# Kernel tuning notes

Measured on AMD Instinct MI355X. Metric: run time of the kernel, lower is better.

## Reference

```python
import jax, jax.numpy as jnp
import numpy as np

N = 500000
E = 1000000
B = 16384
F_IN, H, D = 82, 128, 256


def setup_inputs() -> dict:
    key = jax.random.key(0)
    ks = jax.random.split(key, 12)
    x = jax.random.normal(ks[0], (N, F_IN), dtype=jnp.float32)
    edge_index = jax.random.randint(ks[1], (2, E), 0, N, dtype=jnp.int64)
    batch = jnp.sort(jax.random.randint(ks[2], (N,), 0, B, dtype=jnp.int64))
    s = 0.05
    return {
        "x": x,
        "edge_index": edge_index,
        "batch": batch,
        "W0": jax.random.normal(ks[3], (F_IN, H), dtype=jnp.float32) * s,
        "b0": jnp.zeros((H,), dtype=jnp.float32),
        "W1": jax.random.normal(ks[4], (H, H), dtype=jnp.float32) * s,
        "b1": jnp.zeros((H,), dtype=jnp.float32),
        "W2": jax.random.normal(ks[5], (H, H), dtype=jnp.float32) * s,
        "b2": jnp.zeros((H,), dtype=jnp.float32),
        "gate_w": jax.random.normal(ks[6], (H, 1), dtype=jnp.float32) * s,
        "gate_b": jnp.zeros((1,), dtype=jnp.float32),
        "proj_w": jax.random.normal(ks[7], (H, D), dtype=jnp.float32) * s,
        "proj_b": jnp.zeros((D,), dtype=jnp.float32),
    }


def _gcn_conv(x, src, dst, norm, W, b):
    # PyG GCNConv: linear transform, gather from src, scale by sym-norm, scatter-add to dst
    h = x @ W  # (N, out)
    msg = h[src] * norm[:, None]  # (E+N, out)
    out = jax.ops.segment_sum(msg, dst, num_segments=N)
    return out + b


def reference(x, edge_index, batch, W0, b0, W1, b1, W2, b2, gate_w, gate_b, proj_w, proj_b):
    # add self-loops (GCNConv default add_self_loops=True)
    loop = jnp.arange(N, dtype=edge_index.dtype)
    src = jnp.concatenate([edge_index[0], loop])
    dst = jnp.concatenate([edge_index[1], loop])
    # symmetric normalization: deg computed on target (col) with unit edge weights
    deg = jax.ops.segment_sum(jnp.ones_like(dst, dtype=x.dtype), dst, num_segments=N)
    dis = jnp.where(deg > 0, jax.lax.rsqrt(jnp.maximum(deg, 1.0)), 0.0)
    norm = dis[src] * dis[dst]  # (E+N,)

    h = jax.nn.relu(_gcn_conv(x, src, dst, norm, W0, b0))
    h = jax.nn.relu(_gcn_conv(h, src, dst, norm, W1, b1))
    h = jax.nn.relu(_gcn_conv(h, src, dst, norm, W2, b2))

    # GlobalAttention pooling: segment softmax over gate scores, weighted scatter-sum
    gate = (h @ gate_w + gate_b)[:, 0]  # (N,)
    m = jax.ops.segment_max(gate, batch, num_segments=B)
    e = jnp.exp(gate - m[batch])
    denom = jax.ops.segment_sum(e, batch, num_segments=B)
    alpha = e / denom[batch]  # (N,)
    graph_emb = jax.ops.segment_sum(alpha[:, None] * h, batch, num_segments=B)  # (B, H)

    return graph_emb @ proj_w + proj_b  # (B, D)
```

## Files before the change

kernel.cpp:

```cpp
#include <hip/hip_runtime.h>
#include <hip/hip_bf16.h>
#include <cstdint>


typedef __attribute__((ext_vector_type(8))) short short8;
typedef __attribute__((ext_vector_type(4))) float f32x4;

__device__ __forceinline__ float b2f(unsigned int hi16) {
    return __builtin_bit_cast(float, hi16);
}
__device__ __forceinline__ unsigned short f2b(float f) {
    unsigned int u = __builtin_bit_cast(unsigned int, f);
    u += 0x7fffu + ((u >> 16) & 1u);
    return (unsigned short)(u >> 16);
}
__device__ __forceinline__ unsigned int packbf(float lo, float hi) {
    return ((unsigned int)f2b(hi) << 16) | f2b(lo);
}

__global__ void k_count(const int* __restrict__ dst, int* __restrict__ cnt, int E) {
    int e = blockIdx.x * blockDim.x + threadIdx.x;
    if (e < E) atomicAdd(&cnt[dst[e]], 1);
}

__global__ void k_scan1(const int* __restrict__ in, int* __restrict__ out1,
                        int* __restrict__ bsum, float* __restrict__ dis, int n) {
    __shared__ int s[256];
    int t = threadIdx.x;
    int base = blockIdx.x * 2048 + t * 8;
    int v[8];
    int run = 0;
#pragma unroll
    for (int i = 0; i < 8; ++i) {
        int idx = base + i;
        int x = (idx < n) ? in[idx] : 0;
        if (idx < n) dis[idx] = rsqrtf((float)x + 1.0f);
        run += x;
        v[i] = run;
    }
    s[t] = run;
    __syncthreads();
    for (int off = 1; off < 256; off <<= 1) {
        int add = (t >= off) ? s[t - off] : 0;
        __syncthreads();
        s[t] += add;
        __syncthreads();
    }
    int pre = (t > 0) ? s[t - 1] : 0;
#pragma unroll
    for (int i = 0; i < 8; ++i) {
        int idx = base + i;
        if (idx < n) out1[idx] = v[i] + pre;
    }
    if (t == 255) bsum[blockIdx.x] = s[255];
}

__global__ void k_scan2(int* bsum, int nb) {
    __shared__ int s[256];
    int t = threadIdx.x;
    s[t] = (t < nb) ? bsum[t] : 0;
    __syncthreads();
    for (int off = 1; off < 256; off <<= 1) {
        int add = (t >= off) ? s[t - off] : 0;
        __syncthreads();
        s[t] += add;
        __syncthreads();
    }
    if (t < nb) bsum[t] = s[t];
}

__global__ void k_scan3(int* __restrict__ rowstart, const int* __restrict__ bsum, int n) {
    int b = blockIdx.x, t = threadIdx.x;
    if (b == 0) {
        if (t == 0) rowstart[0] = 0;
        return;
    }
    int add = bsum[b - 1];
    int* out1 = rowstart + 1;
    int base = b * 2048 + t * 8;
#pragma unroll
    for (int i = 0; i < 8; ++i) {
        int idx = base + i;
        if (idx < n) out1[idx] += add;
    }
}

__global__ void k_fill(const int* __restrict__ src, const int* __restrict__ dst,
                       const int* __restrict__ rowstart, int* __restrict__ cur0,
                       int* __restrict__ csr_src, int E) {
    int e = blockIdx.x * blockDim.x + threadIdx.x;
    if (e >= E) return;
    int d = dst[e];
    int pos = rowstart[d] + atomicAdd(&cur0[d], 1);
    csr_src[pos] = src[e];
}

__global__ void k_cvtw3(const float* __restrict__ W0, const float* __restrict__ W1,
                        const float* __restrict__ W2, unsigned short* __restrict__ wp0,
                        unsigned short* __restrict__ wp1, unsigned short* __restrict__ wp2) {
    int tid = blockIdx.x * blockDim.x + threadIdx.x;
    const float* W;
    unsigned short* o;
    int Ksrc, f;
    if (tid < 3 * 512) { W = W0; o = wp0; Ksrc = 82; f = tid; }
    else if (tid < 7 * 512) { W = W1; o = wp1; Ksrc = 128; f = tid - 3 * 512; }
    else if (tid < 11 * 512) { W = W2; o = wp2; Ksrc = 128; f = tid - 7 * 512; }
    else return;
    int lane = f & 63, fr = f >> 6;
    int m = fr >> 3, ct = fr & 7;
    int col = ct * 16 + (lane & 15);
    int kb = m * 32 + ((lane >> 4) << 3);
    unsigned short v[8];
#pragma unroll
    for (int j = 0; j < 8; ++j) {
        int k = kb + j;
        v[j] = (k < Ksrc) ? f2b(W[k * 128 + col]) : (unsigned short)0;
    }
    *(short8*)(o + (size_t)f * 8) = *(short8*)v;
}

__global__ __launch_bounds__(256) void k_xd(const float* __restrict__ x,
                                            const float* __restrict__ dis,
                                            unsigned int* __restrict__ xd, int n) {
    int tid = blockIdx.x * blockDim.x + threadIdx.x;
    if (tid >= n * 48) return;
    int v = tid / 48;
    int c = (tid - v * 48) * 2;
    float dv = dis[v];
    const float* xv = x + (size_t)v * 82;
    float fx = (c < 82) ? dv * xv[c] : 0.f;
    float fy = (c + 1 < 82) ? dv * xv[c + 1] : 0.f;
    xd[tid] = packbf(fx, fy);
}

template <int KS, bool SCALE, bool GATE>
__global__ __launch_bounds__(256, 6) void k_fused(
    const unsigned int* __restrict__ hd, const float* __restrict__ dis,
    const int* __restrict__ rowstart, const int* __restrict__ csr,
    const unsigned short* __restrict__ Wp, const float* __restrict__ bias,
    unsigned short* __restrict__ out, const float* __restrict__ gw,
    const float* __restrict__ gb, float* __restrict__ gate, int n) {
    constexpr int RU = KS * 16;
    __shared__ unsigned int As[64 * 64];
    int t = threadIdx.x, lane = t & 63, w = t >> 6;
    int tile = blockIdx.x * 64;
    const bool act = (RU == 64) ? true : (lane < RU);
    const int li = act ? lane : 0;

    for (int g = 0; g < 4; ++g) {
        int r = (w << 4) + g * 4;
        int v0 = tile + r;
        unsigned int* dst0 = &As[(r + 0) * 64 + (lane ^ (((r + 0) & 7) << 2))];
        unsigned int* dst1 = &As[(r + 1) * 64 + (lane ^ (((r + 1) & 7) << 2))];
        unsigned int* dst2 = &As[(r + 2) * 64 + (lane ^ (((r + 2) & 7) << 2))];
        unsigned int* dst3 = &As[(r + 3) * 64 + (lane ^ (((r + 3) & 7) << 2))];
        if (v0 >= n) {
            *dst0 = 0u; *dst1 = 0u; *dst2 = 0u; *dst3 = 0u;
            continue;
        }
        int nv = n - v0;
        if (nv > 4) nv = 4;
        int e0 = rowstart[v0];
        int eE = rowstart[v0 + nv];
        int b1 = (nv > 1) ? rowstart[v0 + 1] : eE;
        int b2 = (nv > 2) ? rowstart[v0 + 2] : eE;
        int b3 = (nv > 3) ? rowstart[v0 + 3] : eE;

        unsigned int s0 = hd[(size_t)v0 * RU + li];
        unsigned int s1 = (nv > 1) ? hd[(size_t)(v0 + 1) * RU + li] : 0u;
        unsigned int s2 = (nv > 2) ? hd[(size_t)(v0 + 2) * RU + li] : 0u;
        unsigned int s3 = (nv > 3) ? hd[(size_t)(v0 + 3) * RU + li] : 0u;
        float a0x = b2f(s0 << 16), a0y = b2f(s0 & 0xffff0000u);
        float a1x = b2f(s1 << 16), a1y = b2f(s1 & 0xffff0000u);
        float a2x = b2f(s2 << 16), a2y = b2f(s2 & 0xffff0000u);
        float a3x = b2f(s3 << 16), a3y = b2f(s3 & 0xffff0000u);

        for (int e = e0; e < eE; e += 8) {
            int rem = eE - e;
            int i1 = (rem > 1) ? e + 1 : e;
            int i2 = (rem > 2) ? e + 2 : e;
            int i3 = (rem > 3) ? e + 3 : e;
            int i4 = (rem > 4) ? e + 4 : e;
            int i5 = (rem > 5) ? e + 5 : e;
            int i6 = (rem > 6) ? e + 6 : e;
            int i7 = (rem > 7) ? e + 7 : e;
            int u0 = csr[e],  u1 = csr[i1], u2 = csr[i2], u3 = csr[i3];
            int u4 = csr[i4], u5 = csr[i5], u6 = csr[i6], u7 = csr[i7];
            unsigned int r0v = hd[(size_t)u0 * RU + li];
            unsigned int r1v = hd[(size_t)u1 * RU + li];
            unsigned int r2v = hd[(size_t)u2 * RU + li];
            unsigned int r3v = hd[(size_t)u3 * RU + li];
            unsigned int r4v = hd[(size_t)u4 * RU + li];
            unsigned int r5v = hd[(size_t)u5 * RU + li];
            unsigned int r6v = hd[(size_t)u6 * RU + li];
            unsigned int r7v = hd[(size_t)u7 * RU + li];
#define ACC(rv, ei)                                                     \
            {                                                           \
                float fx = b2f((rv) << 16), fy = b2f((rv) & 0xffff0000u); \
                if ((ei) < b1) { a0x += fx; a0y += fy; }                \
                else if ((ei) < b2) { a1x += fx; a1y += fy; }           \
                else if ((ei) < b3) { a2x += fx; a2y += fy; }           \
                else { a3x += fx; a3y += fy; }                          \
            }
            ACC(r0v, e)
            if (rem > 1) ACC(r1v, e + 1)
            if (rem > 2) ACC(r2v, e + 2)
            if (rem > 3) ACC(r3v, e + 3)
            if (rem > 4) ACC(r4v, e + 4)
            if (rem > 5) ACC(r5v, e + 5)
            if (rem > 6) ACC(r6v, e + 6)
            if (rem > 7) ACC(r7v, e + 7)
#undef ACC
        }

        float d0 = dis[v0];
        float d1 = (nv > 1) ? dis[v0 + 1] : 0.f;
        float d2 = (nv > 2) ? dis[v0 + 2] : 0.f;
        float d3 = (nv > 3) ? dis[v0 + 3] : 0.f;
        *dst0 = act ? packbf(d0 * a0x, d0 * a0y) : 0u;
        *dst1 = (act && nv > 1) ? packbf(d1 * a1x, d1 * a1y) : 0u;
        *dst2 = (act && nv > 2) ? packbf(d2 * a2x, d2 * a2y) : 0u;
        *dst3 = (act && nv > 3) ? packbf(d3 * a3x, d3 * a3y) : 0u;
    }
    __syncthreads();

    int r0 = lane & 15, ch = lane >> 4;
    const unsigned int* arow = &As[((w << 4) + r0) << 6];
    f32x4 acc[8];
#pragma unroll
    for (int ct = 0; ct < 8; ++ct) acc[ct] = (f32x4){0.f, 0.f, 0.f, 0.f};
#pragma unroll
    for (int m = 0; m < KS; ++m) {
        int slot = (ch + 4 * m) ^ (r0 & 7);
        short8 a = *(const short8*)(arow + slot * 4);
        const short8* wf = (const short8*)Wp + ((size_t)(m * 8) * 64 + lane);
#pragma unroll
        for (int ct = 0; ct < 8; ++ct) {
            short8 b = wf[ct * 64];
            acc[ct] = __builtin_amdgcn_mfma_f32_16x16x32_bf16(a, b, acc[ct], 0, 0, 0);
        }
    }

    int cq = r0;
    float bb[8], gwv[8];
#pragma unroll
    for (int ct = 0; ct < 8; ++ct) {
        bb[ct] = bias[ct * 16 + cq];
        if (GATE) gwv[ct] = gw[ct * 16 + cq];
    }
    float gbv = GATE ? gb[0] : 0.f;
    int rbase = tile + (w << 4) + (ch << 2);
#pragma unroll
    for (int reg = 0; reg < 4; ++reg) {
        int row = rbase + reg;
        bool ok = row < n;
        float dv = (SCALE && ok) ? dis[row] : 1.f;
        float gp = 0.f;
#pragma unroll
        for (int ct = 0; ct < 8; ++ct) {
            float o = fmaxf(acc[ct][reg] + bb[ct], 0.f);
            if (GATE) gp = fmaf(o, gwv[ct], gp);
            if (ok) out[(size_t)row * 128 + ct * 16 + cq] = f2b(SCALE ? o * dv : o);
        }
        if (GATE) {
            gp += __shfl_xor(gp, 1);
            gp += __shfl_xor(gp, 2);
            gp += __shfl_xor(gp, 4);
            gp += __shfl_xor(gp, 8);
            if (cq == 0 && ok) gate[row] = gp + gbv;
        }
    }
}

__global__ __launch_bounds__(256) void k_pool(const unsigned short* __restrict__ h,
                                              const float* __restrict__ gate,
                                              const int* __restrict__ batch,
                                              float* __restrict__ emb, int n, int B) {
    int wid = (blockIdx.x * blockDim.x + threadIdx.x) >> 6;
    int lane = threadIdx.x & 63;
    if (wid >= B) return;
    int bnd = 0;
    if (lane < 2) {
        int g = wid + lane;
        int lo = 0, hi = n;
        while (lo < hi) {
            int mid = (lo + hi) >> 1;
            if (batch[mid] < g) lo = mid + 1;
            else hi = mid;
        }
        bnd = lo;
    }
    int s = __shfl(bnd, 0), e2 = __shfl(bnd, 1);
    float* ev2 = emb + (size_t)wid * 128 + lane * 2;
    if (s >= e2) {
        ev2[0] = 0.f;
        ev2[1] = 0.f;
        return;
    }
    float m = -INFINITY;
    for (int v = s + lane; v < e2; v += 64) m = fmaxf(m, gate[v]);
#pragma unroll
    for (int off = 32; off; off >>= 1) m = fmaxf(m, __shfl_xor(m, off));
    float a0 = 0.f, a1 = 0.f, den = 0.f;
    for (int v = s; v < e2; ++v) {
        float ev = __expf(gate[v] - m);
        den += ev;
        unsigned int hv = *(const unsigned int*)((const char*)h + (size_t)v * 256 + lane * 4);
        a0 = fmaf(ev, b2f(hv << 16), a0);
        a1 = fmaf(ev, b2f(hv & 0xffff0000u), a1);
    }
    float inv = 1.f / den;
    ev2[0] = a0 * inv;
    ev2[1] = a1 * inv;
}

__global__ __launch_bounds__(256) void k_proj(const float* __restrict__ emb,
                                              const float* __restrict__ pw,
                                              const float* __restrict__ pb,
                                              float* __restrict__ out, int B) {
    __shared__ float es[32][128];
    int g0 = blockIdx.x * 32;
    int t = threadIdx.x;
    for (int i = t; i < 1024; i += 256) {
        int g = g0 + (i >> 5);
        float4 val = (g < B) ? ((const float4*)emb)[(size_t)g * 32 + (i & 31)]
                             : make_float4(0.f, 0.f, 0.f, 0.f);
        *(float4*)&es[i >> 5][(i & 31) * 4] = val;
    }
    __syncthreads();
    float acc[32];
#pragma unroll
    for (int i = 0; i < 32; ++i) acc[i] = 0.f;
    for (int k = 0; k < 128; ++k) {
        float wv = pw[k * 256 + t];
#pragma unroll
        for (int i = 0; i < 32; ++i) acc[i] = fmaf(es[i][k], wv, acc[i]);
    }
    float b = pb[t];
#pragma unroll
    for (int i = 0; i < 32; ++i) {
        int g = g0 + i;
        if (g < B) out[(size_t)g * 256 + t] = acc[i] + b;
    }
}

extern "C" void kernel_launch(void* const* d_in, const int* in_sizes, int n_in,
                              void* d_out, int out_size, void* d_ws, size_t ws_size,
                              hipStream_t stream) {
    const float* x = (const float*)d_in[0];
    const int* ei = (const int*)d_in[1];
    const int* batch = (const int*)d_in[2];
    const float* W0 = (const float*)d_in[3];
    const float* b0 = (const float*)d_in[4];
    const float* W1 = (const float*)d_in[5];
    const float* b1 = (const float*)d_in[6];
    const float* W2 = (const float*)d_in[7];
    const float* b2 = (const float*)d_in[8];
    const float* gw = (const float*)d_in[9];
    const float* gb = (const float*)d_in[10];
    const float* pw = (const float*)d_in[11];
    const float* pb = (const float*)d_in[12];
    float* out = (float*)d_out;

    const int N = in_sizes[2];
    const int E = in_sizes[1] / 2;
    const int B = out_size / 256;
    (void)n_in;

    const int* esrc = ei;
    const int* edst = ei + E;

    char* p = (char*)d_ws;
    auto carve = [&](size_t bytes) {
        char* r = p;
        p += (bytes + 255) & ~(size_t)255;
        return r;
    };
    unsigned int* xd = (unsigned int*)carve((size_t)N * 48 * 4);
    unsigned int* hA = (unsigned int*)carve((size_t)N * 64 * 4);
    unsigned int* hB = (unsigned int*)carve((size_t)N * 64 * 4);
    float* emb = (float*)carve((size_t)B * 128 * 4);
    int* csr_src = (int*)carve((size_t)E * 4);
    float* dis = (float*)carve((size_t)N * 4);
    int* cnt = (int*)carve((size_t)2 * N * 4);
    int* cur0 = cnt + N;
    int* rowstart = (int*)carve((size_t)(N + 1) * 4);
    float* gate = (float*)carve((size_t)N * 4);
    int* bsum = (int*)carve((size_t)4096 * 4);
    unsigned short* wp0 = (unsigned short*)carve((size_t)3 * 512 * 8 * 2);
    unsigned short* wp1 = (unsigned short*)carve((size_t)4 * 512 * 8 * 2);
    unsigned short* wp2 = (unsigned short*)carve((size_t)4 * 512 * 8 * 2);
    if ((size_t)(p - (char*)d_ws) > ws_size) return;

    const int nb = (N + 2047) / 2048;

    hipMemsetAsync(cnt, 0, (size_t)2 * N * 4, stream);
    k_count<<<(E + 255) / 256, 256, 0, stream>>>(edst, cnt, E);
    k_scan1<<<nb, 256, 0, stream>>>(cnt, rowstart + 1, bsum, dis, N);
    k_scan2<<<1, 256, 0, stream>>>(bsum, nb);
    k_scan3<<<nb, 256, 0, stream>>>(rowstart, bsum, N);
    k_fill<<<(E + 255) / 256, 256, 0, stream>>>(esrc, edst, rowstart, cur0, csr_src, E);
    k_cvtw3<<<22, 256, 0, stream>>>(W0, W1, W2, wp0, wp1, wp2);
    k_xd<<<(N * 48 + 255) / 256, 256, 0, stream>>>(x, dis, xd, N);

    const int fb = (N + 63) / 64;

    k_fused<3, true, false><<<fb, 256, 0, stream>>>(
        xd, dis, rowstart, csr_src, wp0, b0, (unsigned short*)hA,
        nullptr, nullptr, nullptr, N);
    k_fused<4, true, false><<<fb, 256, 0, stream>>>(
        hA, dis, rowstart, csr_src, wp1, b1, (unsigned short*)hB,
        nullptr, nullptr, nullptr, N);
    k_fused<4, false, true><<<fb, 256, 0, stream>>>(
        hB, dis, rowstart, csr_src, wp2, b2, (unsigned short*)hA,
        gw, gb, gate, N);

    k_pool<<<(B + 3) / 4, 256, 0, stream>>>((const unsigned short*)hA, gate, batch,
                                            emb, N, B);
    k_proj<<<(B + 31) / 32, 256, 0, stream>>>(emb, pw, pb, out, B);
}
```

Before: 684.4 us.

## Fuse input scaling into first GCN layer and merge scan kernels

Removes the separate k_xd pre-pass: the first layer now gathers fp32 x rows directly and applies the per-source degree scale with fmaf, instead of reading a bf16 pre-scaled copy. This drops one full pass over x and the xd buffer, in exchange for wider fp32 gathers plus extra dis[] gathers per edge. k_scan2 is folded into k_scan3, with each block reducing the block sums itself, which removes one launch. Row starts and self features are prefetched into registers, and the later layers use launch bounds of 8 instead of 6, which adds register pressure.

```diff
diff --git a/kernel.cpp b/kernel.cpp
--- a/kernel.cpp
+++ b/kernel.cpp
@@ -55,27 +55,19 @@
     if (t == 255) bsum[blockIdx.x] = s[255];
 }
 
-__global__ void k_scan2(int* bsum, int nb) {
-    __shared__ int s[256];
-    int t = threadIdx.x;
-    s[t] = (t < nb) ? bsum[t] : 0;
-    __syncthreads();
-    for (int off = 1; off < 256; off <<= 1) {
-        int add = (t >= off) ? s[t - off] : 0;
-        __syncthreads();
-        s[t] += add;
-        __syncthreads();
-    }
-    if (t < nb) bsum[t] = s[t];
-}
-
 __global__ void k_scan3(int* __restrict__ rowstart, const int* __restrict__ bsum, int n) {
     int b = blockIdx.x, t = threadIdx.x;
     if (b == 0) {
         if (t == 0) rowstart[0] = 0;
         return;
     }
-    int add = bsum[b - 1];
+    __shared__ int ws[4];
+    int v = (t < b) ? bsum[t] : 0;
+#pragma unroll
+    for (int off = 32; off; off >>= 1) v += __shfl_xor(v, off);
+    if ((t & 63) == 0) ws[t >> 6] = v;
+    __syncthreads();
+    int add = ws[0] + ws[1] + ws[2] + ws[3];
     int* out1 = rowstart + 1;
     int base = b * 2048 + t * 8;
 #pragma unroll
@@ -119,34 +111,26 @@
     *(short8*)(o + (size_t)f * 8) = *(short8*)v;
 }
 
-__global__ __launch_bounds__(256) void k_xd(const float* __restrict__ x,
-                                            const float* __restrict__ dis,
-                                            unsigned int* __restrict__ xd, int n) {
-    int tid = blockIdx.x * blockDim.x + threadIdx.x;
-    if (tid >= n * 48) return;
-    int v = tid / 48;
-    int c = (tid - v * 48) * 2;
-    float dv = dis[v];
-    const float* xv = x + (size_t)v * 82;
-    float fx = (c < 82) ? dv * xv[c] : 0.f;
-    float fy = (c + 1 < 82) ? dv * xv[c + 1] : 0.f;
-    xd[tid] = packbf(fx, fy);
-}
-
-template <int KS, bool SCALE, bool GATE>
-__global__ __launch_bounds__(256, 6) void k_fused(
-    const unsigned int* __restrict__ hd, const float* __restrict__ dis,
+__global__ __launch_bounds__(256, 6) void k_fused0(
+    const float* __restrict__ x, const float* __restrict__ dis,
     const int* __restrict__ rowstart, const int* __restrict__ csr,
     const unsigned short* __restrict__ Wp, const float* __restrict__ bias,
-    unsigned short* __restrict__ out, const float* __restrict__ gw,
-    const float* __restrict__ gb, float* __restrict__ gate, int n) {
-    constexpr int RU = KS * 16;
+    unsigned short* __restrict__ out, int n) {
     __shared__ unsigned int As[64 * 64];
     int t = threadIdx.x, lane = t & 63, w = t >> 6;
     int tile = blockIdx.x * 64;
-    const bool act = (RU == 64) ? true : (lane < RU);
-    const int li = act ? lane : 0;
-
+    const bool act = lane < 41;
+    const int c0 = (act ? lane : 0) * 2;
+    int sbase = tile + (w << 4);
+
+    int bb[17];
+#pragma unroll
+    for (int i = 0; i < 17; ++i) {
+        int idx = sbase + i;
+        bb[i] = rowstart[idx < n ? idx : n];
+    }
+
+#pragma unroll
     for (int g = 0; g < 4; ++g) {
         int r = (w << 4) + g * 4;
         int v0 = tile + r;
@@ -154,26 +138,26 @@
         unsigned int* dst1 = &As[(r + 1) * 64 + (lane ^ (((r + 1) & 7) << 2))];
         unsigned int* dst2 = &As[(r + 2) * 64 + (lane ^ (((r + 2) & 7) << 2))];
         unsigned int* dst3 = &As[(r + 3) * 64 + (lane ^ (((r + 3) & 7) << 2))];
-        if (v0 >= n) {
+        int nv = n - v0;
+        nv = nv < 0 ? 0 : (nv > 4 ? 4 : nv);
+        if (nv == 0) {
             *dst0 = 0u; *dst1 = 0u; *dst2 = 0u; *dst3 = 0u;
             continue;
         }
-        int nv = n - v0;
-        if (nv > 4) nv = 4;
-        int e0 = rowstart[v0];
-        int eE = rowstart[v0 + nv];
-        int b1 = (nv > 1) ? rowstart[v0 + 1] : eE;
-        int b2 = (nv > 2) ? rowstart[v0 + 2] : eE;
-        int b3 = (nv > 3) ? rowstart[v0 + 3] : eE;
-
-        unsigned int s0 = hd[(size_t)v0 * RU + li];
-        unsigned int s1 = (nv > 1) ? hd[(size_t)(v0 + 1) * RU + li] : 0u;
-        unsigned int s2 = (nv > 2) ? hd[(size_t)(v0 + 2) * RU + li] : 0u;
-        unsigned int s3 = (nv > 3) ? hd[(size_t)(v0 + 3) * RU + li] : 0u;
-        float a0x = b2f(s0 << 16), a0y = b2f(s0 & 0xffff0000u);
-        float a1x = b2f(s1 << 16), a1y = b2f(s1 & 0xffff0000u);
-        float a2x = b2f(s2 << 16), a2y = b2f(s2 & 0xffff0000u);
-        float a3x = b2f(s3 << 16), a3y = b2f(s3 & 0xffff0000u);
+        int e0 = bb[g * 4], b1 = bb[g * 4 + 1], b2 = bb[g * 4 + 2],
+            b3 = bb[g * 4 + 3], eE = bb[g * 4 + 4];
+        int vc1 = (nv > 1) ? v0 + 1 : v0;
+        int vc2 = (nv > 2) ? v0 + 2 : v0;
+        int vc3 = (nv > 3) ? v0 + 3 : v0;
+        float2 t0 = *(const float2*)(x + (size_t)v0 * 82 + c0);
+        float2 t1 = *(const float2*)(x + (size_t)vc1 * 82 + c0);
+        float2 t2 = *(const float2*)(x + (size_t)vc2 * 82 + c0);
+        float2 t3 = *(const float2*)(x + (size_t)vc3 * 82 + c0);
+        float d0 = dis[v0], d1 = dis[vc1], d2 = dis[vc2], d3 = dis[vc3];
+        float a0x = d0 * t0.x, a0y = d0 * t0.y;
+        float a1x = d1 * t1.x, a1y = d1 * t1.y;
+        float a2x = d2 * t2.x, a2y = d2 * t2.y;
+        float a3x = d3 * t3.x, a3y = d3 * t3.y;
 
         for (int e = e0; e < eE; e += 8) {
             int rem = eE - e;
@@ -186,14 +170,137 @@
             int i7 = (rem > 7) ? e + 7 : e;
             int u0 = csr[e],  u1 = csr[i1], u2 = csr[i2], u3 = csr[i3];
             int u4 = csr[i4], u5 = csr[i5], u6 = csr[i6], u7 = csr[i7];
-            unsigned int r0v = hd[(size_t)u0 * RU + li];
-            unsigned int r1v = hd[(size_t)u1 * RU + li];
-            unsigned int r2v = hd[(size_t)u2 * RU + li];
-            unsigned int r3v = hd[(size_t)u3 * RU + li];
-            unsigned int r4v = hd[(size_t)u4 * RU + li];
-            unsigned int r5v = hd[(size_t)u5 * RU + li];
-            unsigned int r6v = hd[(size_t)u6 * RU + li];
-            unsigned int r7v = hd[(size_t)u7 * RU + li];
+            float2 r0 = *(const float2*)(x + (size_t)u0 * 82 + c0);
+            float2 r1 = *(const float2*)(x + (size_t)u1 * 82 + c0);
+            float2 r2 = *(const float2*)(x + (size_t)u2 * 82 + c0);
+            float2 r3 = *(const float2*)(x + (size_t)u3 * 82 + c0);
+            float2 r4 = *(const float2*)(x + (size_t)u4 * 82 + c0);
+            float2 r5 = *(const float2*)(x + (size_t)u5 * 82 + c0);
+            float2 r6 = *(const float2*)(x + (size_t)u6 * 82 + c0);
+            float2 r7 = *(const float2*)(x + (size_t)u7 * 82 + c0);
+            float du0 = dis[u0], du1 = dis[u1], du2 = dis[u2], du3 = dis[u3];
+            float du4 = dis[u4], du5 = dis[u5], du6 = dis[u6], du7 = dis[u7];
+#define ACC0(DU, RV, ei)                                                  \
+            {                                                             \
+                if ((ei) < b1) { a0x = fmaf(DU, RV.x, a0x); a0y = fmaf(DU, RV.y, a0y); } \
+                else if ((ei) < b2) { a1x = fmaf(DU, RV.x, a1x); a1y = fmaf(DU, RV.y, a1y); } \
+                else if ((ei) < b3) { a2x = fmaf(DU, RV.x, a2x); a2y = fmaf(DU, RV.y, a2y); } \
+                else { a3x = fmaf(DU, RV.x, a3x); a3y = fmaf(DU, RV.y, a3y); } \
+            }
+            ACC0(du0, r0, e)
+            if (rem > 1) ACC0(du1, r1, e + 1)
+            if (rem > 2) ACC0(du2, r2, e + 2)
+            if (rem > 3) ACC0(du3, r3, e + 3)
+            if (rem > 4) ACC0(du4, r4, e + 4)
+            if (rem > 5) ACC0(du5, r5, e + 5)
+            if (rem > 6) ACC0(du6, r6, e + 6)
+            if (rem > 7) ACC0(du7, r7, e + 7)
+#undef ACC0
+        }
+        *dst0 = act ? packbf(d0 * a0x, d0 * a0y) : 0u;
+        *dst1 = (act && nv > 1) ? packbf(d1 * a1x, d1 * a1y) : 0u;
+        *dst2 = (act && nv > 2) ? packbf(d2 * a2x, d2 * a2y) : 0u;
+        *dst3 = (act && nv > 3) ? packbf(d3 * a3x, d3 * a3y) : 0u;
+    }
+    __syncthreads();
+
+    int r0i = lane & 15, ch = lane >> 4;
+    const unsigned int* arow = &As[((w << 4) + r0i) << 6];
+    f32x4 acc[8];
+#pragma unroll
+    for (int ct = 0; ct < 8; ++ct) acc[ct] = (f32x4){0.f, 0.f, 0.f, 0.f};
+#pragma unroll
+    for (int m = 0; m < 3; ++m) {
+        int slot = (ch + 4 * m) ^ (r0i & 7);
+        short8 a = *(const short8*)(arow + slot * 4);
+        const short8* wf = (const short8*)Wp + ((size_t)(m * 8) * 64 + lane);
+#pragma unroll
+        for (int ct = 0; ct < 8; ++ct) {
+            short8 b = wf[ct * 64];
+            acc[ct] = __builtin_amdgcn_mfma_f32_16x16x32_bf16(a, b, acc[ct], 0, 0, 0);
+        }
+    }
+
+    float bbv[8];
+#pragma unroll
+    for (int ct = 0; ct < 8; ++ct) bbv[ct] = bias[ct * 16 + r0i];
+    int rbase = tile + (w << 4) + (ch << 2);
+#pragma unroll
+    for (int reg = 0; reg < 4; ++reg) {
+        int row = rbase + reg;
+        bool ok = row < n;
+        float dv = ok ? dis[row] : 1.f;
+#pragma unroll
+        for (int ct = 0; ct < 8; ++ct) {
+            float o = fmaxf(acc[ct][reg] + bbv[ct], 0.f);
+            if (ok) out[(size_t)row * 128 + ct * 16 + r0i] = f2b(o * dv);
+        }
+    }
+}
+
+template <bool SCALE, bool GATE>
+__global__ __launch_bounds__(256, 8) void k_fused(
+    const unsigned int* __restrict__ hd, const float* __restrict__ dis,
+    const int* __restrict__ rowstart, const int* __restrict__ csr,
+    const unsigned short* __restrict__ Wp, const float* __restrict__ bias,
+    unsigned short* __restrict__ out, const float* __restrict__ gw,
+    const float* __restrict__ gb, float* __restrict__ gate, int n) {
+    __shared__ unsigned int As[64 * 64];
+    int t = threadIdx.x, lane = t & 63, w = t >> 6;
+    int tile = blockIdx.x * 64;
+    int sbase = tile + (w << 4);
+
+    int bb[17];
+#pragma unroll
+    for (int i = 0; i < 17; ++i) {
+        int idx = sbase + i;
+        bb[i] = rowstart[idx < n ? idx : n];
+    }
+    unsigned int selfv[16];
+#pragma unroll
+    for (int i = 0; i < 16; ++i) {
+        int v = sbase + i;
+        int vc = (v < n) ? v : 0;
+        unsigned int val = hd[(size_t)vc * 64 + lane];
+        selfv[i] = (v < n) ? val : 0u;
+    }
+
+#pragma unroll
+    for (int g = 0; g < 4; ++g) {
+        int r = (w << 4) + g * 4;
+        int v0 = tile + r;
+        unsigned int* dst0 = &As[(r + 0) * 64 + (lane ^ (((r + 0) & 7) << 2))];
+        unsigned int* dst1 = &As[(r + 1) * 64 + (lane ^ (((r + 1) & 7) << 2))];
+        unsigned int* dst2 = &As[(r + 2) * 64 + (lane ^ (((r + 2) & 7) << 2))];
+        unsigned int* dst3 = &As[(r + 3) * 64 + (lane ^ (((r + 3) & 7) << 2))];
+        int nv = n - v0;
+        nv = nv < 0 ? 0 : (nv > 4 ? 4 : nv);
+        int e0 = bb[g * 4], b1 = bb[g * 4 + 1], b2 = bb[g * 4 + 2],
+            b3 = bb[g * 4 + 3], eE = bb[g * 4 + 4];
+        float a0x = b2f(selfv[g * 4 + 0] << 16), a0y = b2f(selfv[g * 4 + 0] & 0xffff0000u);
+        float a1x = b2f(selfv[g * 4 + 1] << 16), a1y = b2f(selfv[g * 4 + 1] & 0xffff0000u);
+        float a2x = b2f(selfv[g * 4 + 2] << 16), a2y = b2f(selfv[g * 4 + 2] & 0xffff0000u);
+        float a3x = b2f(selfv[g * 4 + 3] << 16), a3y = b2f(selfv[g * 4 + 3] & 0xffff0000u);
+
+        for (int e = e0; e < eE; e += 8) {
+            int rem = eE - e;
+            int i1 = (rem > 1) ? e + 1 : e;
+            int i2 = (rem > 2) ? e + 2 : e;
+            int i3 = (rem > 3) ? e + 3 : e;
+            int i4 = (rem > 4) ? e + 4 : e;
+            int i5 = (rem > 5) ? e + 5 : e;
+            int i6 = (rem > 6) ? e + 6 : e;
+            int i7 = (rem > 7) ? e + 7 : e;
+            int u0 = csr[e],  u1 = csr[i1], u2 = csr[i2], u3 = csr[i3];
+            int u4 = csr[i4], u5 = csr[i5], u6 = csr[i6], u7 = csr[i7];
+            unsigned int r0v = hd[(size_t)u0 * 64 + lane];
+            unsigned int r1v = hd[(size_t)u1 * 64 + lane];
+            unsigned int r2v = hd[(size_t)u2 * 64 + lane];
+            unsigned int r3v = hd[(size_t)u3 * 64 + lane];
+            unsigned int r4v = hd[(size_t)u4 * 64 + lane];
+            unsigned int r5v = hd[(size_t)u5 * 64 + lane];
+            unsigned int r6v = hd[(size_t)u6 * 64 + lane];
+            unsigned int r7v = hd[(size_t)u7 * 64 + lane];
 #define ACC(rv, ei)                                                     \
             {                                                           \
                 float fx = b2f((rv) << 16), fy = b2f((rv) & 0xffff0000u); \
@@ -213,25 +320,26 @@
 #undef ACC
         }
 
-        float d0 = dis[v0];
-        float d1 = (nv > 1) ? dis[v0 + 1] : 0.f;
-        float d2 = (nv > 2) ? dis[v0 + 2] : 0.f;
-        float d3 = (nv > 3) ? dis[v0 + 3] : 0.f;
-        *dst0 = act ? packbf(d0 * a0x, d0 * a0y) : 0u;
-        *dst1 = (act && nv > 1) ? packbf(d1 * a1x, d1 * a1y) : 0u;
-        *dst2 = (act && nv > 2) ? packbf(d2 * a2x, d2 * a2y) : 0u;
-        *dst3 = (act && nv > 3) ? packbf(d3 * a3x, d3 * a3y) : 0u;
+        int vc1 = (nv > 1) ? v0 + 1 : 0;
+        int vc2 = (nv > 2) ? v0 + 2 : 0;
+        int vc3 = (nv > 3) ? v0 + 3 : 0;
+        float d0 = dis[(nv > 0) ? v0 : 0];
+        float d1 = dis[vc1], d2 = dis[vc2], d3 = dis[vc3];
+        *dst0 = (nv > 0) ? packbf(d0 * a0x, d0 * a0y) : 0u;
+        *dst1 = (nv > 1) ? packbf(d1 * a1x, d1 * a1y) : 0u;
+        *dst2 = (nv > 2) ? packbf(d2 * a2x, d2 * a2y) : 0u;
+        *dst3 = (nv > 3) ? packbf(d3 * a3x, d3 * a3y) : 0u;
     }
     __syncthreads();
 
-    int r0 = lane & 15, ch = lane >> 4;
-    const unsigned int* arow = &As[((w << 4) + r0) << 6];
+    int r0i = lane & 15, ch = lane >> 4;
+    const unsigned int* arow = &As[((w << 4) + r0i) << 6];
     f32x4 acc[8];
 #pragma unroll
     for (int ct = 0; ct < 8; ++ct) acc[ct] = (f32x4){0.f, 0.f, 0.f, 0.f};
 #pragma unroll
-    for (int m = 0; m < KS; ++m) {
-        int slot = (ch + 4 * m) ^ (r0 & 7);
+    for (int m = 0; m < 4; ++m) {
+        int slot = (ch + 4 * m) ^ (r0i & 7);
         short8 a = *(const short8*)(arow + slot * 4);
         const short8* wf = (const short8*)Wp + ((size_t)(m * 8) * 64 + lane);
 #pragma unroll
@@ -241,12 +349,11 @@
         }
     }
 
-    int cq = r0;
-    float bb[8], gwv[8];
+    float bbv[8], gwv[8];
 #pragma unroll
     for (int ct = 0; ct < 8; ++ct) {
-        bb[ct] = bias[ct * 16 + cq];
-        if (GATE) gwv[ct] = gw[ct * 16 + cq];
+        bbv[ct] = bias[ct * 16 + r0i];
+        if (GATE) gwv[ct] = gw[ct * 16 + r0i];
     }
     float gbv = GATE ? gb[0] : 0.f;
     int rbase = tile + (w << 4) + (ch << 2);
@@ -258,16 +365,16 @@
         float gp = 0.f;
 #pragma unroll
         for (int ct = 0; ct < 8; ++ct) {
-            float o = fmaxf(acc[ct][reg] + bb[ct], 0.f);
+            float o = fmaxf(acc[ct][reg] + bbv[ct], 0.f);
             if (GATE) gp = fmaf(o, gwv[ct], gp);
-            if (ok) out[(size_t)row * 128 + ct * 16 + cq] = f2b(SCALE ? o * dv : o);
+            if (ok) out[(size_t)row * 128 + ct * 16 + r0i] = f2b(SCALE ? o * dv : o);
         }
         if (GATE) {
             gp += __shfl_xor(gp, 1);
             gp += __shfl_xor(gp, 2);
             gp += __shfl_xor(gp, 4);
             gp += __shfl_xor(gp, 8);
-            if (cq == 0 && ok) gate[row] = gp + gbv;
+            if (r0i == 0 && ok) gate[row] = gp + gbv;
         }
     }
 }
@@ -376,7 +483,6 @@
         p += (bytes + 255) & ~(size_t)255;
         return r;
     };
-    unsigned int* xd = (unsigned int*)carve((size_t)N * 48 * 4);
     unsigned int* hA = (unsigned int*)carve((size_t)N * 64 * 4);
     unsigned int* hB = (unsigned int*)carve((size_t)N * 64 * 4);
     float* emb = (float*)carve((size_t)B * 128 * 4);
@@ -397,21 +503,18 @@
     hipMemsetAsync(cnt, 0, (size_t)2 * N * 4, stream);
     k_count<<<(E + 255) / 256, 256, 0, stream>>>(edst, cnt, E);
     k_scan1<<<nb, 256, 0, stream>>>(cnt, rowstart + 1, bsum, dis, N);
-    k_scan2<<<1, 256, 0, stream>>>(bsum, nb);
     k_scan3<<<nb, 256, 0, stream>>>(rowstart, bsum, N);
     k_fill<<<(E + 255) / 256, 256, 0, stream>>>(esrc, edst, rowstart, cur0, csr_src, E);
     k_cvtw3<<<22, 256, 0, stream>>>(W0, W1, W2, wp0, wp1, wp2);
-    k_xd<<<(N * 48 + 255) / 256, 256, 0, stream>>>(x, dis, xd, N);
 
     const int fb = (N + 63) / 64;
 
-    k_fused<3, true, false><<<fb, 256, 0, stream>>>(
-        xd, dis, rowstart, csr_src, wp0, b0, (unsigned short*)hA,
-        nullptr, nullptr, nullptr, N);
-    k_fused<4, true, false><<<fb, 256, 0, stream>>>(
+    k_fused0<<<fb, 256, 0, stream>>>(x, dis, rowstart, csr_src, wp0, b0,
+                                     (unsigned short*)hA, N);
+    k_fused<true, false><<<fb, 256, 0, stream>>>(
         hA, dis, rowstart, csr_src, wp1, b1, (unsigned short*)hB,
         nullptr, nullptr, nullptr, N);
-    k_fused<4, false, true><<<fb, 256, 0, stream>>>(
+    k_fused<false, true><<<fb, 256, 0, stream>>>(
         hB, dis, rowstart, csr_src, wp2, b2, (unsigned short*)hA,
         gw, gb, gate, N);
 
```

Measured after the change: 827.7 us. 20.9% more time.

## Use single-wave blocks in fused GCN kernel, fold scan2 into scan3, unroll pooling

Applied to the files above, without the earlier changes.

The fused gather+MFMA kernel now runs one wave per block over 16 rows instead of four waves over 64 rows, dropping the block barrier and letting waves finish independently of slower siblings. The second scan pass is folded into the third by having each block reduce preceding block sums itself, removing a launch. The attention pooling loop is unrolled by four to overlap loads of gate and features. Smaller blocks mean more block scheduling and a different occupancy limit from the new launch bounds.

```diff
diff --git a/kernel.cpp b/kernel.cpp
--- a/kernel.cpp
+++ b/kernel.cpp
@@ -55,27 +55,19 @@
     if (t == 255) bsum[blockIdx.x] = s[255];
 }
 
-__global__ void k_scan2(int* bsum, int nb) {
-    __shared__ int s[256];
-    int t = threadIdx.x;
-    s[t] = (t < nb) ? bsum[t] : 0;
-    __syncthreads();
-    for (int off = 1; off < 256; off <<= 1) {
-        int add = (t >= off) ? s[t - off] : 0;
-        __syncthreads();
-        s[t] += add;
-        __syncthreads();
-    }
-    if (t < nb) bsum[t] = s[t];
-}
-
 __global__ void k_scan3(int* __restrict__ rowstart, const int* __restrict__ bsum, int n) {
     int b = blockIdx.x, t = threadIdx.x;
     if (b == 0) {
         if (t == 0) rowstart[0] = 0;
         return;
     }
-    int add = bsum[b - 1];
+    __shared__ int ws[4];
+    int v = (t < b) ? bsum[t] : 0;
+#pragma unroll
+    for (int off = 32; off; off >>= 1) v += __shfl_xor(v, off);
+    if ((t & 63) == 0) ws[t >> 6] = v;
+    __syncthreads();
+    int add = ws[0] + ws[1] + ws[2] + ws[3];
     int* out1 = rowstart + 1;
     int base = b * 2048 + t * 8;
 #pragma unroll
@@ -134,21 +126,21 @@
 }
 
 template <int KS, bool SCALE, bool GATE>
-__global__ __launch_bounds__(256, 6) void k_fused(
+__global__ __launch_bounds__(64, 8) void k_fused(
     const unsigned int* __restrict__ hd, const float* __restrict__ dis,
     const int* __restrict__ rowstart, const int* __restrict__ csr,
     const unsigned short* __restrict__ Wp, const float* __restrict__ bias,
     unsigned short* __restrict__ out, const float* __restrict__ gw,
     const float* __restrict__ gb, float* __restrict__ gate, int n) {
     constexpr int RU = KS * 16;
-    __shared__ unsigned int As[64 * 64];
-    int t = threadIdx.x, lane = t & 63, w = t >> 6;
-    int tile = blockIdx.x * 64;
+    __shared__ unsigned int As[16 * 64];
+    int lane = threadIdx.x & 63;
+    int tile = blockIdx.x * 16;
     const bool act = (RU == 64) ? true : (lane < RU);
     const int li = act ? lane : 0;
 
     for (int g = 0; g < 4; ++g) {
-        int r = (w << 4) + g * 4;
+        int r = g * 4;
         int v0 = tile + r;
         unsigned int* dst0 = &As[(r + 0) * 64 + (lane ^ (((r + 0) & 7) << 2))];
         unsigned int* dst1 = &As[(r + 1) * 64 + (lane ^ (((r + 1) & 7) << 2))];
@@ -222,10 +214,9 @@
         *dst2 = (act && nv > 2) ? packbf(d2 * a2x, d2 * a2y) : 0u;
         *dst3 = (act && nv > 3) ? packbf(d3 * a3x, d3 * a3y) : 0u;
     }
-    __syncthreads();
 
     int r0 = lane & 15, ch = lane >> 4;
-    const unsigned int* arow = &As[((w << 4) + r0) << 6];
+    const unsigned int* arow = &As[r0 << 6];
     f32x4 acc[8];
 #pragma unroll
     for (int ct = 0; ct < 8; ++ct) acc[ct] = (f32x4){0.f, 0.f, 0.f, 0.f};
@@ -241,15 +232,14 @@
         }
     }
 
-    int cq = r0;
     float bb[8], gwv[8];
 #pragma unroll
     for (int ct = 0; ct < 8; ++ct) {
-        bb[ct] = bias[ct * 16 + cq];
-        if (GATE) gwv[ct] = gw[ct * 16 + cq];
+        bb[ct] = bias[ct * 16 + r0];
+        if (GATE) gwv[ct] = gw[ct * 16 + r0];
     }
     float gbv = GATE ? gb[0] : 0.f;
-    int rbase = tile + (w << 4) + (ch << 2);
+    int rbase = tile + (ch << 2);
 #pragma unroll
     for (int reg = 0; reg < 4; ++reg) {
         int row = rbase + reg;
@@ -260,14 +250,14 @@
         for (int ct = 0; ct < 8; ++ct) {
             float o = fmaxf(acc[ct][reg] + bb[ct], 0.f);
             if (GATE) gp = fmaf(o, gwv[ct], gp);
-            if (ok) out[(size_t)row * 128 + ct * 16 + cq] = f2b(SCALE ? o * dv : o);
+            if (ok) out[(size_t)row * 128 + ct * 16 + r0] = f2b(SCALE ? o * dv : o);
         }
         if (GATE) {
             gp += __shfl_xor(gp, 1);
             gp += __shfl_xor(gp, 2);
             gp += __shfl_xor(gp, 4);
             gp += __shfl_xor(gp, 8);
-            if (cq == 0 && ok) gate[row] = gp + gbv;
+            if (r0 == 0 && ok) gate[row] = gp + gbv;
         }
     }
 }
@@ -302,10 +292,30 @@
 #pragma unroll
     for (int off = 32; off; off >>= 1) m = fmaxf(m, __shfl_xor(m, off));
     float a0 = 0.f, a1 = 0.f, den = 0.f;
-    for (int v = s; v < e2; ++v) {
+    const unsigned int* h32 = (const unsigned int*)h;
+    int v = s;
+    for (; v + 4 <= e2; v += 4) {
+        float g0 = gate[v], g1 = gate[v + 1], g2 = gate[v + 2], g3 = gate[v + 3];
+        unsigned int h0 = h32[(size_t)(v + 0) * 64 + lane];
+        unsigned int h1 = h32[(size_t)(v + 1) * 64 + lane];
+        unsigned int h2 = h32[(size_t)(v + 2) * 64 + lane];
+        unsigned int h3 = h32[(size_t)(v + 3) * 64 + lane];
+        float e0 = __expf(g0 - m), e1 = __expf(g1 - m);
+        float e2v = __expf(g2 - m), e3 = __expf(g3 - m);
+        den += (e0 + e1) + (e2v + e3);
+        a0 = fmaf(e0, b2f(h0 << 16), a0);
+        a1 = fmaf(e0, b2f(h0 & 0xffff0000u), a1);
+        a0 = fmaf(e1, b2f(h1 << 16), a0);
+        a1 = fmaf(e1, b2f(h1 & 0xffff0000u), a1);
+        a0 = fmaf(e2v, b2f(h2 << 16), a0);
+        a1 = fmaf(e2v, b2f(h2 & 0xffff0000u), a1);
+        a0 = fmaf(e3, b2f(h3 << 16), a0);
+        a1 = fmaf(e3, b2f(h3 & 0xffff0000u), a1);
+    }
+    for (; v < e2; ++v) {
         float ev = __expf(gate[v] - m);
         den += ev;
-        unsigned int hv = *(const unsigned int*)((const char*)h + (size_t)v * 256 + lane * 4);
+        unsigned int hv = h32[(size_t)v * 64 + lane];
         a0 = fmaf(ev, b2f(hv << 16), a0);
         a1 = fmaf(ev, b2f(hv & 0xffff0000u), a1);
     }
@@ -397,21 +407,20 @@
     hipMemsetAsync(cnt, 0, (size_t)2 * N * 4, stream);
     k_count<<<(E + 255) / 256, 256, 0, stream>>>(edst, cnt, E);
     k_scan1<<<nb, 256, 0, stream>>>(cnt, rowstart + 1, bsum, dis, N);
-    k_scan2<<<1, 256, 0, stream>>>(bsum, nb);
     k_scan3<<<nb, 256, 0, stream>>>(rowstart, bsum, N);
     k_fill<<<(E + 255) / 256, 256, 0, stream>>>(esrc, edst, rowstart, cur0, csr_src, E);
     k_cvtw3<<<22, 256, 0, stream>>>(W0, W1, W2, wp0, wp1, wp2);
     k_xd<<<(N * 48 + 255) / 256, 256, 0, stream>>>(x, dis, xd, N);
 
-    const int fb = (N + 63) / 64;
-
-    k_fused<3, true, false><<<fb, 256, 0, stream>>>(
+    const int fb = (N + 15) / 16;
+
+    k_fused<3, true, false><<<fb, 64, 0, stream>>>(
         xd, dis, rowstart, csr_src, wp0, b0, (unsigned short*)hA,
         nullptr, nullptr, nullptr, N);
-    k_fused<4, true, false><<<fb, 256, 0, stream>>>(
+    k_fused<4, true, false><<<fb, 64, 0, stream>>>(
         hA, dis, rowstart, csr_src, wp1, b1, (unsigned short*)hB,
         nullptr, nullptr, nullptr, N);
-    k_fused<4, false, true><<<fb, 256, 0, stream>>>(
+    k_fused<4, false, true><<<fb, 64, 0, stream>>>(
         hB, dis, rowstart, csr_src, wp2, b2, (unsigned short*)hA,
         gw, gb, gate, N);
 
```

New measurement: 622.4 us. 1.1x faster.
